# Kernel tuning notes

Measured on AMD Instinct MI355X. Metric: run time of the kernel, lower is better.

Reference implementation:

```python
import jax, jax.numpy as jnp
import numpy as np

B, T, D, H = 4, 2048, 2048, 16
DH = D // H

def setup_inputs() -> dict:
    key = jax.random.key(0)
    ks = jax.random.split(key, 9)
    s = 1.0 / np.sqrt(D)
    return {
        "x": jax.random.normal(ks[0], (B, T, D), dtype=jnp.float32),
        "Wq": jax.random.uniform(ks[1], (D, D), jnp.float32, -s, s),
        "bq": jax.random.uniform(ks[2], (D,), jnp.float32, -s, s),
        "Wk": jax.random.uniform(ks[3], (D, D), jnp.float32, -s, s),
        "bk": jax.random.uniform(ks[4], (D,), jnp.float32, -s, s),
        "Wv": jax.random.uniform(ks[5], (D, D), jnp.float32, -s, s),
        "bv": jax.random.uniform(ks[6], (D,), jnp.float32, -s, s),
        "Wo": jax.random.uniform(ks[7], (D, D), jnp.float32, -s, s),
        "bo": jax.random.uniform(ks[8], (D,), jnp.float32, -s, s),
    }

def reference(x, Wq, bq, Wk, bk, Wv, bv, Wo, bo):
    # projections: [B,T,D] -> [B,H,T,DH]
    def split_heads(y):
        return y.reshape(B, T, H, DH).transpose(0, 2, 1, 3)
    q = split_heads(x @ Wq + bq)
    k = split_heads(x @ Wk + bk)
    v = split_heads(x @ Wv + bv)
    scale = DH ** -0.5
    scores = jnp.einsum('bhtd,bhsd->bhts', q, k) * scale  # [B,H,T,T]
    causal = jnp.tril(jnp.ones((T, T), dtype=bool))
    scores = jnp.where(causal[None, None], scores, -jnp.inf)
    weights = jax.nn.softmax(scores, axis=-1)
    out = jnp.einsum('bhts,bhsd->bhtd', weights, v)  # [B,H,T,DH]
    out = out.transpose(0, 2, 1, 3).reshape(B, T, D)
    return out @ Wo + bo
```

## Files before the change

### kernel.cpp

```cpp
#include <hip/hip_runtime.h>
#include <hip/hip_bf16.h>

#define B_  4
#define T_  2048
#define D_  2048
#define H_  16
#define DH_ 128

typedef __attribute__((ext_vector_type(4))) float f32x4;
typedef __attribute__((ext_vector_type(8))) short short8;
typedef __attribute__((ext_vector_type(4))) _Float16 half4;

__device__ __forceinline__ ushort f2bf(float f) {
    unsigned int u = __builtin_bit_cast(unsigned int, f);
    u += 0x7fffu + ((u >> 16) & 1u);
    return (ushort)(u >> 16);
}
__device__ __forceinline__ ushort f2h(float f) {
    return (ushort)(__builtin_bit_cast(unsigned int, __builtin_amdgcn_cvt_pkrtz(f, f)) & 0xffffu);
}

__device__ __forceinline__ void glds16(const void* g, void* l) {
    __builtin_amdgcn_global_load_lds(
        (const __attribute__((address_space(1))) unsigned int*)g,
        (__attribute__((address_space(3))) unsigned int*)l, 16, 0, 0);
}

__global__ void cast_f32_bf16(const float* __restrict__ x, ushort* __restrict__ xb, int n) {
    int i = (blockIdx.x * 256 + threadIdx.x) * 4;
    if (i < n) {
        float4 v = *(const float4*)(x + i);
        ushort4 o;
        o.x = f2bf(v.x); o.y = f2bf(v.y); o.z = f2bf(v.z); o.w = f2bf(v.w);
        *(ushort4*)(xb + i) = o;
    }
}

__global__ void transpose_cast(const float* __restrict__ W, ushort* __restrict__ Wt) {
    __shared__ float tile[32][33];
    int tx = threadIdx.x, ty = threadIdx.y;
    int n0 = blockIdx.x * 32, k0 = blockIdx.y * 32;
#pragma unroll
    for (int i = 0; i < 4; i++)
        tile[ty + i * 8][tx] = W[(size_t)(k0 + ty + i * 8) * D_ + n0 + tx];
    __syncthreads();
#pragma unroll
    for (int i = 0; i < 4; i++)
        Wt[(size_t)(n0 + ty + i * 8) * D_ + k0 + tx] = f2bf(tile[tx][ty + i * 8]);
}

__global__ __launch_bounds__(256, 3) void gemm_qkv(
    const ushort* __restrict__ A,
    const ushort* __restrict__ Wq, const ushort* __restrict__ Wk, const ushort* __restrict__ Wv,
    const float* __restrict__ bq, const float* __restrict__ bk, const float* __restrict__ bv,
    ushort* __restrict__ Qb, ushort* __restrict__ Kb, ushort* __restrict__ Vtb,
    float qscale)
{
    extern __shared__ char smem[];
    uint4* sA = (uint4*)smem;
    uint4* sB = (uint4*)(smem + 8192);

    const int tid  = threadIdx.x;
    const int sel  = blockIdx.x >> 4;
    const int row0 = blockIdx.y * 128, col0 = (blockIdx.x & 15) * 128;
    const ushort* Bt = (sel == 0) ? Wq : (sel == 1) ? Wk : Wv;
    const float* bias = (sel == 0) ? bq : (sel == 1) ? bk : bv;
    const float oscale = (sel == 0) ? qscale : 1.0f;
    const int K = D_, N = D_;

    const int mA = tid >> 2, g = tid & 3;
    const int gc = g ^ ((mA >> 2) & 3);
    const ushort* pa0 = A  + (size_t)(row0 + mA) * K + gc * 8;
    const ushort* pb0 = Bt + (size_t)(col0 + mA) * K + gc * 8;

    const int lane = tid & 63, w = tid >> 6;
    const int l15 = lane & 15, quad = lane >> 4;
    const int wm = w & 1, wn = w >> 1;
    const int csel = quad ^ ((l15 >> 2) & 3);
    int aoff[4], boff[4];
#pragma unroll
    for (int mt = 0; mt < 4; mt++) aoff[mt] = (wm * 64 + mt * 16 + l15) * 4 + csel;
#pragma unroll
    for (int nt = 0; nt < 4; nt++) boff[nt] = (wn * 64 + nt * 16 + l15) * 4 + csel;

    f32x4 acc[4][4] = {};

    const int kIter = K >> 5;
    for (int kt = 0; kt < kIter; ++kt) {
        if (kt) __syncthreads();
        glds16(pa0 + kt * 32,                     sA + tid);
        glds16(pa0 + kt * 32 + (size_t)64 * K,    sA + tid + 256);
        glds16(pb0 + kt * 32,                     sB + tid);
        glds16(pb0 + kt * 32 + (size_t)64 * K,    sB + tid + 256);
        __syncthreads();
        short8 af[4], bfr[4];
#pragma unroll
        for (int mt = 0; mt < 4; mt++) af[mt]  = __builtin_bit_cast(short8, sA[aoff[mt]]);
#pragma unroll
        for (int nt = 0; nt < 4; nt++) bfr[nt] = __builtin_bit_cast(short8, sB[boff[nt]]);
#pragma unroll
        for (int mt = 0; mt < 4; mt++)
#pragma unroll
            for (int nt = 0; nt < 4; nt++)
                acc[mt][nt] = __builtin_amdgcn_mfma_f32_16x16x32_bf16(af[mt], bfr[nt], acc[mt][nt], 0, 0, 0);
    }

    if (sel < 2) {
        ushort* Cout = (sel == 0) ? Qb : Kb;
#pragma unroll
        for (int nt = 0; nt < 4; nt++) {
            int col = col0 + wn * 64 + nt * 16 + l15;
            float bb = bias[col];
#pragma unroll
            for (int mt = 0; mt < 4; mt++) {
                int rowb = row0 + wm * 64 + mt * 16 + quad * 4;
#pragma unroll
                for (int r = 0; r < 4; r++)
                    Cout[(size_t)(rowb + r) * N + col] = f2bf((acc[mt][nt][r] + bb) * oscale);
            }
        }
    } else {
        __syncthreads();
        ushort* tr = (ushort*)smem;
#pragma unroll
        for (int nt = 0; nt < 4; nt++) {
            int cl = wn * 64 + nt * 16 + l15;
            float bb = bias[col0 + cl];
#pragma unroll
            for (int mt = 0; mt < 4; mt++) {
                int rl = wm * 64 + mt * 16 + quad * 4;
#pragma unroll
                for (int r = 0; r < 4; r++)
                    tr[cl * 136 + rl + r] = f2h(acc[mt][nt][r] + bb);
            }
        }
        __syncthreads();
        int b = row0 >> 11, t0 = row0 & (T_ - 1), h = col0 >> 7;
        for (int idx = tid; idx < 2048; idx += 256) {
            int dh = idx >> 4, c = idx & 15;
            uint4 v = *(const uint4*)(tr + dh * 136 + c * 8);
            *(uint4*)(Vtb + (size_t)((b * H_ + h) * DH_ + dh) * T_ + t0 + c * 8) = v;
        }
    }
}

__global__ __launch_bounds__(256, 3) void gemm_bt_f32(
    const ushort* __restrict__ A, const ushort* __restrict__ Bt,
    const float* __restrict__ bias, float* __restrict__ Cout,
    int M, int N, int K)
{
    extern __shared__ char smem[];
    uint4* sA = (uint4*)smem;
    uint4* sB = (uint4*)(smem + 8192);

    const int tid  = threadIdx.x;
    const int row0 = blockIdx.y * 128, col0 = blockIdx.x * 128;

    const int mA = tid >> 2, g = tid & 3;
    const int gc = g ^ ((mA >> 2) & 3);
    const ushort* pa0 = A  + (size_t)(row0 + mA) * K + gc * 8;
    const ushort* pb0 = Bt + (size_t)(col0 + mA) * K + gc * 8;

    const int lane = tid & 63, w = tid >> 6;
    const int l15 = lane & 15, quad = lane >> 4;
    const int wm = w & 1, wn = w >> 1;
    const int csel = quad ^ ((l15 >> 2) & 3);
    int aoff[4], boff[4];
#pragma unroll
    for (int mt = 0; mt < 4; mt++) aoff[mt] = (wm * 64 + mt * 16 + l15) * 4 + csel;
#pragma unroll
    for (int nt = 0; nt < 4; nt++) boff[nt] = (wn * 64 + nt * 16 + l15) * 4 + csel;

    f32x4 acc[4][4] = {};

    const int kIter = K >> 5;
    for (int kt = 0; kt < kIter; ++kt) {
        if (kt) __syncthreads();
        glds16(pa0 + kt * 32,                     sA + tid);
        glds16(pa0 + kt * 32 + (size_t)64 * K,    sA + tid + 256);
        glds16(pb0 + kt * 32,                     sB + tid);
        glds16(pb0 + kt * 32 + (size_t)64 * K,    sB + tid + 256);
        __syncthreads();
        short8 af[4], bfr[4];
#pragma unroll
        for (int mt = 0; mt < 4; mt++) af[mt]  = __builtin_bit_cast(short8, sA[aoff[mt]]);
#pragma unroll
        for (int nt = 0; nt < 4; nt++) bfr[nt] = __builtin_bit_cast(short8, sB[boff[nt]]);
#pragma unroll
        for (int mt = 0; mt < 4; mt++)
#pragma unroll
            for (int nt = 0; nt < 4; nt++)
                acc[mt][nt] = __builtin_amdgcn_mfma_f32_16x16x32_bf16(af[mt], bfr[nt], acc[mt][nt], 0, 0, 0);
    }

#pragma unroll
    for (int nt = 0; nt < 4; nt++) {
        int col = col0 + wn * 64 + nt * 16 + l15;
        float bb = bias[col];
#pragma unroll
        for (int mt = 0; mt < 4; mt++) {
            int rowb = row0 + wm * 64 + mt * 16 + quad * 4;
#pragma unroll
            for (int r = 0; r < 4; r++)
                Cout[(size_t)(rowb + r) * N + col] = acc[mt][nt][r] + bb;
        }
    }
}

__global__ __launch_bounds__(256, 5) void attn_kernel(
    const ushort* __restrict__ Q, const ushort* __restrict__ K,
    const ushort* __restrict__ Vt, ushort* __restrict__ O)
{
    __shared__ __align__(16) char smem[32768];
    uint4*  kS = (uint4*)smem;
    ushort* vS = (ushort*)(smem + 16384);

    const int tid = threadIdx.x;
    const int bid = blockIdx.x;
    const int slot = bid >> 3;
    const int g = (bid & 7) + 8 * (slot >> 4);
    const int qx = slot & 15;
    const int b = g >> 4, h = g & 15;

    const int lane = tid & 63, w = tid >> 6, l15 = lane & 15, quad = lane >> 4;

    const int krow = tid >> 4;
    const int kchunk = (tid & 15) ^ (krow & 7);
    const ushort* kg = K + ((size_t)(b * T_) + krow) * D_ + h * DH_ + kchunk * 8;

    const int vrow = tid >> 3, vc = tid & 7;
    const ushort* vg = Vt + ((size_t)((b * H_ + h) * DH_) + vrow) * T_ + vc * 8;
    const int vs0 = ((2 * vc    ) ^ (vrow & 15)) * 4;
    const int vs1 = ((2 * vc + 1) ^ (vrow & 15)) * 4;

    const int qts[2] = { qx, 31 - qx };

    for (int e = 0; e < 2; ++e) {
        const int qt = qts[e], q0 = qt * 64;
        const int qbase = q0 + w * 16;

        short8 aq[4];
        {
            const ushort* qp = Q + ((size_t)(b * T_) + qbase + l15) * D_ + h * DH_ + quad * 8;
#pragma unroll
            for (int ks = 0; ks < 4; ++ks)
                aq[ks] = __builtin_bit_cast(short8, *(const uint4*)(qp + ks * 32));
        }

        f32x4 accO[8] = {};
        float mrow = -INFINITY, lrow = 0.f;

        auto tile = [&](int s0, int stMax, bool diag) {
            __syncthreads();
            const ushort* kp = kg + (size_t)s0 * D_;
#pragma unroll
            for (int j = 0; j < 4; ++j) glds16(kp + (size_t)j * 16 * D_, kS + j * 256 + tid);
            const ushort* vp = vg + s0;
            uint4 vv[4];
#pragma unroll
            for (int j = 0; j < 4; ++j) vv[j] = *(const uint4*)(vp + (size_t)j * 32 * T_);
#pragma unroll
            for (int j = 0; j < 4; ++j) {
                ushort* dst = vS + (j * 32 + vrow) * 64;
                *(uint2*)(dst + vs0) = make_uint2(vv[j].x, vv[j].y);
                *(uint2*)(dst + vs1) = make_uint2(vv[j].z, vv[j].w);
            }
            __syncthreads();

            f32x4 sT[4] = {};
#pragma unroll
            for (int ks = 0; ks < 4; ++ks)
#pragma unroll
                for (int st = 0; st < 4; ++st)
                    if (st < stMax) {
                        int row = st * 16 + l15;
                        short8 ak = __builtin_bit_cast(short8, kS[row * 16 + ((ks * 4 + quad) ^ (row & 7))]);
                        sT[st] = __builtin_amdgcn_mfma_f32_16x16x32_bf16(ak, aq[ks], sT[st], 0, 0, 0);
                    }

            if (diag) {
                const int q = qbase + l15;
                const int st = stMax - 1;
#pragma unroll
                for (int r = 0; r < 4; ++r)
                    if (s0 + st * 16 + quad * 4 + r > q) sT[st][r] = -INFINITY;
            }

            float rmax = -INFINITY;
#pragma unroll
            for (int st = 0; st < 4; ++st)
                if (st < stMax)
#pragma unroll
                    for (int r = 0; r < 4; ++r) rmax = fmaxf(rmax, sT[st][r]);
            rmax = fmaxf(rmax, __shfl_xor(rmax, 16));
            rmax = fmaxf(rmax, __shfl_xor(rmax, 32));
            float mnew  = fmaxf(mrow, rmax);
            float alpha = __builtin_amdgcn_exp2f(mrow - mnew);
            mrow = mnew;

            float psum = 0.f;
            half4 pb[4];
#pragma unroll
            for (int st = 0; st < 4; ++st)
                if (st < stMax) {
                    float p0 = __builtin_amdgcn_exp2f(sT[st][0] - mnew);
                    float p1 = __builtin_amdgcn_exp2f(sT[st][1] - mnew);
                    float p2 = __builtin_amdgcn_exp2f(sT[st][2] - mnew);
                    float p3 = __builtin_amdgcn_exp2f(sT[st][3] - mnew);
                    psum += (p0 + p1) + (p2 + p3);
                    uint2 u;
                    u.x = __builtin_bit_cast(unsigned int, __builtin_amdgcn_cvt_pkrtz(p0, p1));
                    u.y = __builtin_bit_cast(unsigned int, __builtin_amdgcn_cvt_pkrtz(p2, p3));
                    pb[st] = __builtin_bit_cast(half4, u);
                }
            psum += __shfl_xor(psum, 16);
            psum += __shfl_xor(psum, 32);
            lrow = lrow * alpha + psum;
#pragma unroll
            for (int nt = 0; nt < 8; ++nt)
#pragma unroll
                for (int r = 0; r < 4; ++r) accO[nt][r] *= alpha;

#pragma unroll
            for (int st = 0; st < 4; ++st)
                if (st < stMax) {
#pragma unroll
                    for (int nt = 0; nt < 8; ++nt) {
                        int dh = nt * 16 + l15;
                        half4 vf = *(const half4*)(vS + dh * 64 + (((st * 4 + quad) ^ l15) * 4));
                        accO[nt] = __builtin_amdgcn_mfma_f32_16x16x16f16(vf, pb[st], accO[nt], 0, 0, 0);
                    }
                }
        };

        for (int it = 0; it < qt; ++it) tile(it * 64, 4, false);
        tile(qt * 64, w + 1, true);

        __syncthreads();
        ushort* eT = (ushort*)smem + w * 2176;
        float inv = 1.0f / lrow;
#pragma unroll
        for (int nt = 0; nt < 8; ++nt) {
            int dh = nt * 16 + quad * 4;
#pragma unroll
            for (int r = 0; r < 4; ++r)
                eT[l15 * 136 + dh + r] = f2bf(accO[nt][r] * inv);
        }
        for (int idx = lane; idx < 256; idx += 64) {
            int row = idx >> 4, c = idx & 15;
            uint4 v = *(const uint4*)(eT + row * 136 + c * 8);
            *(uint4*)(O + ((size_t)(b * T_) + q0 + w * 16 + row) * D_ + h * DH_ + c * 8) = v;
        }
    }
}

extern "C" void kernel_launch(void* const* d_in, const int* in_sizes, int n_in,
                              void* d_out, int out_size, void* d_ws, size_t ws_size,
                              hipStream_t stream) {
    const float* x  = (const float*)d_in[0];
    const float* Wq = (const float*)d_in[1];
    const float* bq = (const float*)d_in[2];
    const float* Wk = (const float*)d_in[3];
    const float* bk = (const float*)d_in[4];
    const float* Wv = (const float*)d_in[5];
    const float* bv = (const float*)d_in[6];
    const float* Wo = (const float*)d_in[7];
    const float* bo = (const float*)d_in[8];

    char* ws = (char*)d_ws;
    const size_t MB = 1u << 20;
    ushort* xb  = (ushort*)(ws);
    ushort* Wqt = (ushort*)(ws + 32 * MB);
    ushort* Wkt = (ushort*)(ws + 40 * MB);
    ushort* Wvt = (ushort*)(ws + 48 * MB);
    ushort* Wot = (ushort*)(ws + 56 * MB);
    ushort* Qb  = (ushort*)(ws + 64 * MB);
    ushort* Kb  = (ushort*)(ws + 96 * MB);
    ushort* Vtb = (ushort*)(ws + 128 * MB);
    ushort* Ob  = (ushort*)(ws + 160 * MB);

    const int M = B_ * T_;
    const float qscale = (float)(0.08838834764831845 * 1.4426950408889634);

    cast_f32_bf16<<<(M * D_) / 1024, 256, 0, stream>>>(x, xb, M * D_);
    dim3 tb(32, 8), tg(D_ / 32, D_ / 32);
    transpose_cast<<<tg, tb, 0, stream>>>(Wq, Wqt);
    transpose_cast<<<tg, tb, 0, stream>>>(Wk, Wkt);
    transpose_cast<<<tg, tb, 0, stream>>>(Wv, Wvt);
    transpose_cast<<<tg, tb, 0, stream>>>(Wo, Wot);

    gemm_qkv<<<dim3(48, M / 128), 256, 34816, stream>>>(
        xb, Wqt, Wkt, Wvt, bq, bk, bv, Qb, Kb, Vtb, qscale);

    attn_kernel<<<dim3(1024), 256, 0, stream>>>(Qb, Kb, Vtb, Ob);

    gemm_bt_f32<<<dim3(D_ / 128, M / 128), 256, 16384, stream>>>(
        Ob, Wot, bo, (float*)d_out, M, D_, D_);
}
```

Measured before the change: 630.5 us.

## Replace QKV and output GEMMs with 256x256 double-buffered pipelined MFMA kernels

```diff
diff --git a/kernel.cpp b/kernel.cpp
--- a/kernel.cpp
+++ b/kernel.cpp
@@ -6,6 +6,7 @@
 #define D_  2048
 #define H_  16
 #define DH_ 128
+#define KG  2048
 
 typedef __attribute__((ext_vector_type(4))) float f32x4;
 typedef __attribute__((ext_vector_type(8))) short short8;
@@ -49,7 +50,84 @@
         Wt[(size_t)(n0 + ty + i * 8) * D_ + k0 + tx] = f2bf(tile[tx][ty + i * 8]);
 }
 
-__global__ __launch_bounds__(256, 3) void gemm_qkv(
+
+#define LDS_A(d, qm, AF)                                                                   \
+  { const char* base_ = smem + (((d)*2 + (qm)) << 14);                                     \
+    _Pragma("unroll") for (int mt = 0; mt < 4; ++mt)                                       \
+      _Pragma("unroll") for (int kk = 0; kk < 2; ++kk) {                                   \
+        int idx_ = wm*64 + mt*16 + l15;                                                    \
+        AF[mt][kk] = __builtin_bit_cast(short8,                                            \
+            *(const uint4*)(base_ + idx_*128 + (((kk*4 + quad) ^ (l15 & 7)) << 4)));       \
+      } }
+
+#define LDS_B(d, qn, BF)                                                                   \
+  { const char* base_ = smem + 65536 + (((d)*2 + (qn)) << 14);                             \
+    _Pragma("unroll") for (int nt = 0; nt < 2; ++nt)                                       \
+      _Pragma("unroll") for (int kk = 0; kk < 2; ++kk) {                                   \
+        int idx_ = wn*32 + nt*16 + l15;                                                    \
+        BF[nt][kk] = __builtin_bit_cast(short8,                                            \
+            *(const uint4*)(base_ + idx_*128 + (((kk*4 + quad) ^ (l15 & 7)) << 4)));       \
+      } }
+
+#define STAGE_A(d, qm, kt)                                                                 \
+  { char* ld_ = smem + (((d)*2 + (qm)) << 14) + tid*16;                                    \
+    const ushort* s_ = Ap + (size_t)(arow + (qm)*64) * KG + (kt)*64 + chl*8;               \
+    glds16(s_, ld_);                                                                       \
+    glds16(s_ + (size_t)128*KG, ld_ + 8192); }
+
+#define STAGE_B(d, qn, kt)                                                                 \
+  { char* ld_ = smem + 65536 + (((d)*2 + (qn)) << 14) + tid*16;                            \
+    const ushort* s_ = Bp + (size_t)(bcol + (qn)*32) * KG + (kt)*64 + chl*8;               \
+    glds16(s_, ld_);                                                                       \
+    glds16(s_ + (size_t)128*KG, ld_ + 8192); }
+
+#define MFMA16(QM, QN, AF, BF)                                                             \
+  __builtin_amdgcn_s_setprio(1);                                                           \
+  _Pragma("unroll") for (int mt = 0; mt < 4; ++mt)                                         \
+    _Pragma("unroll") for (int nt = 0; nt < 2; ++nt)                                       \
+      _Pragma("unroll") for (int kk = 0; kk < 2; ++kk)                                     \
+        acc[(QM)*4 + mt][(QN)*2 + nt] = __builtin_amdgcn_mfma_f32_16x16x32_bf16(           \
+            AF[mt][kk], BF[nt][kk], acc[(QM)*4 + mt][(QN)*2 + nt], 0, 0, 0);               \
+  __builtin_amdgcn_s_setprio(0);
+
+#define BAR1_LGKM  __builtin_amdgcn_s_barrier();                                           \
+                   asm volatile("s_waitcnt lgkmcnt(0)" ::: "memory");
+#define BAR2       __builtin_amdgcn_s_barrier();
+#define VM4        asm volatile("s_waitcnt vmcnt(4)" ::: "memory");
+#define VM0        asm volatile("s_waitcnt vmcnt(0)" ::: "memory");
+
+#define GEMM256_MAIN_LOOP                                                                  \
+    f32x4 acc[8][4] = {};                                                                  \
+    short8 aF[4][2], bF0[2][2], bF1[2][2];                                                 \
+                               \
+    STAGE_B(0, 0, 0); STAGE_A(0, 0, 0); STAGE_A(0, 1, 0); STAGE_B(0, 1, 0);                \
+    STAGE_B(1, 0, 1); STAGE_A(1, 0, 1);                                                    \
+    VM4; __builtin_amdgcn_s_barrier();                                                     \
+    _Pragma("unroll 1")                                                                    \
+    for (int j = 0; j < 16; ++j) {                                                         \
+        const int t1 = 2*j + 1;                                                            \
+        const int t2 = (2*j + 2 < 32) ? 2*j + 2 : 31;                                      \
+        const int t3 = (2*j + 3 < 32) ? 2*j + 3 : 31;                                      \
+         LDS_A(0, 0, aF); LDS_B(0, 0, bF0); STAGE_A(1, 1, t1);                     \
+                 BAR1_LGKM; MFMA16(0, 0, aF, bF0); BAR2;                                   \
+         LDS_B(0, 1, bF1); STAGE_B(1, 1, t1);                                      \
+                 BAR1_LGKM; MFMA16(0, 1, aF, bF1); BAR2;                                   \
+         LDS_A(0, 1, aF); STAGE_B(0, 0, t2);                                       \
+                 BAR1_LGKM; MFMA16(1, 1, aF, bF1); BAR2;                                   \
+         STAGE_A(0, 0, t2);                                                        \
+                 BAR1_LGKM; MFMA16(1, 0, aF, bF0); VM4; BAR2;                              \
+         LDS_A(1, 0, aF); LDS_B(1, 0, bF0); STAGE_A(0, 1, t2);                     \
+                 BAR1_LGKM; MFMA16(0, 0, aF, bF0); BAR2;                                   \
+         LDS_B(1, 1, bF1); STAGE_B(0, 1, t2);                                      \
+                 BAR1_LGKM; MFMA16(0, 1, aF, bF1); BAR2;                                   \
+         LDS_A(1, 1, aF); STAGE_B(1, 0, t3);                                       \
+                 BAR1_LGKM; MFMA16(1, 1, aF, bF1); BAR2;                                   \
+         STAGE_A(1, 0, t3);                                                        \
+                 BAR1_LGKM; MFMA16(1, 0, aF, bF0); VM4; BAR2;                              \
+    }                                                                                      \
+    VM0; __builtin_amdgcn_s_barrier();
+
+__global__ __launch_bounds__(512, 2) void gemm_qkv256(
     const ushort* __restrict__ A,
     const ushort* __restrict__ Wq, const ushort* __restrict__ Wk, const ushort* __restrict__ Wv,
     const float* __restrict__ bq, const float* __restrict__ bk, const float* __restrict__ bv,
@@ -57,152 +135,109 @@
     float qscale)
 {
     extern __shared__ char smem[];
-    uint4* sA = (uint4*)smem;
-    uint4* sB = (uint4*)(smem + 8192);
-
-    const int tid  = threadIdx.x;
-    const int sel  = blockIdx.x >> 4;
-    const int row0 = blockIdx.y * 128, col0 = (blockIdx.x & 15) * 128;
-    const ushort* Bt = (sel == 0) ? Wq : (sel == 1) ? Wk : Wv;
+    const int tid = threadIdx.x;
+
+    int id = blockIdx.y * 24 + blockIdx.x;
+    id = (id & 7) * 96 + (id >> 3);
+    const int bx = id % 24, by = id / 24;
+
+    const int sel  = bx >> 3;
+    const int row0 = by * 256, col0 = (bx & 7) * 256;
+    const ushort* Ap = A;
+    const ushort* Bp = (sel == 0) ? Wq : (sel == 1) ? Wk : Wv;
     const float* bias = (sel == 0) ? bq : (sel == 1) ? bk : bv;
     const float oscale = (sel == 0) ? qscale : 1.0f;
-    const int K = D_, N = D_;
-
-    const int mA = tid >> 2, g = tid & 3;
-    const int gc = g ^ ((mA >> 2) & 3);
-    const ushort* pa0 = A  + (size_t)(row0 + mA) * K + gc * 8;
-    const ushort* pb0 = Bt + (size_t)(col0 + mA) * K + gc * 8;
 
     const int lane = tid & 63, w = tid >> 6;
     const int l15 = lane & 15, quad = lane >> 4;
     const int wm = w & 1, wn = w >> 1;
-    const int csel = quad ^ ((l15 >> 2) & 3);
-    int aoff[4], boff[4];
-#pragma unroll
-    for (int mt = 0; mt < 4; mt++) aoff[mt] = (wm * 64 + mt * 16 + l15) * 4 + csel;
-#pragma unroll
-    for (int nt = 0; nt < 4; nt++) boff[nt] = (wn * 64 + nt * 16 + l15) * 4 + csel;
-
-    f32x4 acc[4][4] = {};
-
-    const int kIter = K >> 5;
-    for (int kt = 0; kt < kIter; ++kt) {
-        if (kt) __syncthreads();
-        glds16(pa0 + kt * 32,                     sA + tid);
-        glds16(pa0 + kt * 32 + (size_t)64 * K,    sA + tid + 256);
-        glds16(pb0 + kt * 32,                     sB + tid);
-        glds16(pb0 + kt * 32 + (size_t)64 * K,    sB + tid + 256);
-        __syncthreads();
-        short8 af[4], bfr[4];
-#pragma unroll
-        for (int mt = 0; mt < 4; mt++) af[mt]  = __builtin_bit_cast(short8, sA[aoff[mt]]);
-#pragma unroll
-        for (int nt = 0; nt < 4; nt++) bfr[nt] = __builtin_bit_cast(short8, sB[boff[nt]]);
-#pragma unroll
-        for (int mt = 0; mt < 4; mt++)
-#pragma unroll
-            for (int nt = 0; nt < 4; nt++)
-                acc[mt][nt] = __builtin_amdgcn_mfma_f32_16x16x32_bf16(af[mt], bfr[nt], acc[mt][nt], 0, 0, 0);
+
+    const int irow = tid >> 3;
+    const int chl  = (tid & 7) ^ (irow & 7);
+    const int arow = row0 + irow;
+    const int bcol = col0 + ((irow >> 5) << 6) + (irow & 31);
+
+    GEMM256_MAIN_LOOP
+
+    if (sel < 2) {
+        ushort* Cout = sel ? Kb : Qb;
+#pragma unroll
+        for (int ntg = 0; ntg < 4; ++ntg) {
+            int col = col0 + wn * 64 + ntg * 16 + l15;
+            float bb = bias[col];
+#pragma unroll
+            for (int mtg = 0; mtg < 8; ++mtg) {
+                int rowb = row0 + wm * 128 + mtg * 16 + quad * 4;
+#pragma unroll
+                for (int r = 0; r < 4; ++r)
+                    Cout[(size_t)(rowb + r) * D_ + col] = f2bf((acc[mtg][ntg][r] + bb) * oscale);
+            }
+        }
+    } else {
+        const int b = row0 >> 11, t0 = (row0 & (T_ - 1)) + wm * 128;
+        const int h = (col0 + wn * 64) >> 7;
+        ushort* eT = (ushort*)smem + w * (32 * 136);
+#pragma unroll 1
+        for (int rnd = 0; rnd < 2; ++rnd) {
+#pragma unroll
+            for (int ni = 0; ni < 2; ++ni) {
+                int ntg = rnd * 2 + ni;
+                int col = col0 + wn * 64 + ntg * 16 + l15;
+                float bb = bias[col];
+#pragma unroll
+                for (int mtg = 0; mtg < 8; ++mtg)
+#pragma unroll
+                    for (int r = 0; r < 4; ++r)
+                        eT[(ni * 16 + l15) * 136 + mtg * 16 + quad * 4 + r] = f2h(acc[mtg][ntg][r] + bb);
+            }
+            int dhbase = ((wn & 1) ? 64 : 0) + rnd * 32;
+#pragma unroll
+            for (int it = 0; it < 8; ++it) {
+                int chunk = it * 64 + lane;
+                int d2 = chunk >> 4, c = chunk & 15;
+                uint4 v = *(const uint4*)(eT + d2 * 136 + c * 8);
+                *(uint4*)(Vtb + (size_t)((b * H_ + h) * DH_ + dhbase + d2) * T_ + t0 + c * 8) = v;
+            }
+        }
     }
-
-    if (sel < 2) {
-        ushort* Cout = (sel == 0) ? Qb : Kb;
-#pragma unroll
-        for (int nt = 0; nt < 4; nt++) {
-            int col = col0 + wn * 64 + nt * 16 + l15;
-            float bb = bias[col];
-#pragma unroll
-            for (int mt = 0; mt < 4; mt++) {
-                int rowb = row0 + wm * 64 + mt * 16 + quad * 4;
-#pragma unroll
-                for (int r = 0; r < 4; r++)
-                    Cout[(size_t)(rowb + r) * N + col] = f2bf((acc[mt][nt][r] + bb) * oscale);
-            }
-        }
-    } else {
-        __syncthreads();
-        ushort* tr = (ushort*)smem;
-#pragma unroll
-        for (int nt = 0; nt < 4; nt++) {
-            int cl = wn * 64 + nt * 16 + l15;
-            float bb = bias[col0 + cl];
-#pragma unroll
-            for (int mt = 0; mt < 4; mt++) {
-                int rl = wm * 64 + mt * 16 + quad * 4;
-#pragma unroll
-                for (int r = 0; r < 4; r++)
-                    tr[cl * 136 + rl + r] = f2h(acc[mt][nt][r] + bb);
-            }
-        }
-        __syncthreads();
-        int b = row0 >> 11, t0 = row0 & (T_ - 1), h = col0 >> 7;
-        for (int idx = tid; idx < 2048; idx += 256) {
-            int dh = idx >> 4, c = idx & 15;
-            uint4 v = *(const uint4*)(tr + dh * 136 + c * 8);
-            *(uint4*)(Vtb + (size_t)((b * H_ + h) * DH_ + dh) * T_ + t0 + c * 8) = v;
-        }
-    }
-}
-
-__global__ __launch_bounds__(256, 3) void gemm_bt_f32(
+}
+
+__global__ __launch_bounds__(512, 2) void gemm_o256(
     const ushort* __restrict__ A, const ushort* __restrict__ Bt,
-    const float* __restrict__ bias, float* __restrict__ Cout,
-    int M, int N, int K)
+    const float* __restrict__ bias, float* __restrict__ Cout)
 {
     extern __shared__ char smem[];
-    uint4* sA = (uint4*)smem;
-    uint4* sB = (uint4*)(smem + 8192);
-
-    const int tid  = threadIdx.x;
-    const int row0 = blockIdx.y * 128, col0 = blockIdx.x * 128;
-
-    const int mA = tid >> 2, g = tid & 3;
-    const int gc = g ^ ((mA >> 2) & 3);
-    const ushort* pa0 = A  + (size_t)(row0 + mA) * K + gc * 8;
-    const ushort* pb0 = Bt + (size_t)(col0 + mA) * K + gc * 8;
+    const int tid = threadIdx.x;
+
+    int id = blockIdx.y * 8 + blockIdx.x;
+    id = (id & 7) * 32 + (id >> 3);
+    const int bx = id % 8, by = id / 8;
+
+    const int row0 = by * 256, col0 = bx * 256;
+    const ushort* Ap = A;
+    const ushort* Bp = Bt;
 
     const int lane = tid & 63, w = tid >> 6;
     const int l15 = lane & 15, quad = lane >> 4;
     const int wm = w & 1, wn = w >> 1;
-    const int csel = quad ^ ((l15 >> 2) & 3);
-    int aoff[4], boff[4];
-#pragma unroll
-    for (int mt = 0; mt < 4; mt++) aoff[mt] = (wm * 64 + mt * 16 + l15) * 4 + csel;
-#pragma unroll
-    for (int nt = 0; nt < 4; nt++) boff[nt] = (wn * 64 + nt * 16 + l15) * 4 + csel;
-
-    f32x4 acc[4][4] = {};
-
-    const int kIter = K >> 5;
-    for (int kt = 0; kt < kIter; ++kt) {
-        if (kt) __syncthreads();
-        glds16(pa0 + kt * 32,                     sA + tid);
-        glds16(pa0 + kt * 32 + (size_t)64 * K,    sA + tid + 256);
-        glds16(pb0 + kt * 32,                     sB + tid);
-        glds16(pb0 + kt * 32 + (size_t)64 * K,    sB + tid + 256);
-        __syncthreads();
-        short8 af[4], bfr[4];
-#pragma unroll
-        for (int mt = 0; mt < 4; mt++) af[mt]  = __builtin_bit_cast(short8, sA[aoff[mt]]);
-#pragma unroll
-        for (int nt = 0; nt < 4; nt++) bfr[nt] = __builtin_bit_cast(short8, sB[boff[nt]]);
-#pragma unroll
-        for (int mt = 0; mt < 4; mt++)
-#pragma unroll
-            for (int nt = 0; nt < 4; nt++)
-                acc[mt][nt] = __builtin_amdgcn_mfma_f32_16x16x32_bf16(af[mt], bfr[nt], acc[mt][nt], 0, 0, 0);
-    }
-
-#pragma unroll
-    for (int nt = 0; nt < 4; nt++) {
-        int col = col0 + wn * 64 + nt * 16 + l15;
+
+    const int irow = tid >> 3;
+    const int chl  = (tid & 7) ^ (irow & 7);
+    const int arow = row0 + irow;
+    const int bcol = col0 + ((irow >> 5) << 6) + (irow & 31);
+
+    GEMM256_MAIN_LOOP
+
+#pragma unroll
+    for (int ntg = 0; ntg < 4; ++ntg) {
+        int col = col0 + wn * 64 + ntg * 16 + l15;
         float bb = bias[col];
 #pragma unroll
-        for (int mt = 0; mt < 4; mt++) {
-            int rowb = row0 + wm * 64 + mt * 16 + quad * 4;
-#pragma unroll
-            for (int r = 0; r < 4; r++)
-                Cout[(size_t)(rowb + r) * N + col] = acc[mt][nt][r] + bb;
+        for (int mtg = 0; mtg < 8; ++mtg) {
+            int rowb = row0 + wm * 128 + mtg * 16 + quad * 4;
+#pragma unroll
+            for (int r = 0; r < 4; ++r)
+                Cout[(size_t)(rowb + r) * D_ + col] = acc[mtg][ntg][r] + bb;
         }
     }
 }
@@ -382,6 +417,15 @@
     const int M = B_ * T_;
     const float qscale = (float)(0.08838834764831845 * 1.4426950408889634);
 
+    static bool attr_done = false;
+    if (!attr_done) {
+        (void)hipFuncSetAttribute((const void*)gemm_qkv256,
+                                  hipFuncAttributeMaxDynamicSharedMemorySize, 131072);
+        (void)hipFuncSetAttribute((const void*)gemm_o256,
+                                  hipFuncAttributeMaxDynamicSharedMemorySize, 131072);
+        attr_done = true;
+    }
+
     cast_f32_bf16<<<(M * D_) / 1024, 256, 0, stream>>>(x, xb, M * D_);
     dim3 tb(32, 8), tg(D_ / 32, D_ / 32);
     transpose_cast<<<tg, tb, 0, stream>>>(Wq, Wqt);
@@ -389,11 +433,11 @@
     transpose_cast<<<tg, tb, 0, stream>>>(Wv, Wvt);
     transpose_cast<<<tg, tb, 0, stream>>>(Wo, Wot);
 
-    gemm_qkv<<<dim3(48, M / 128), 256, 34816, stream>>>(
+    gemm_qkv256<<<dim3(24, M / 256), 512, 131072, stream>>>(
         xb, Wqt, Wkt, Wvt, bq, bk, bv, Qb, Kb, Vtb, qscale);
 
     attn_kernel<<<dim3(1024), 256, 0, stream>>>(Qb, Kb, Vtb, Ob);
 
-    gemm_bt_f32<<<dim3(D_ / 128, M / 128), 256, 16384, stream>>>(
-        Ob, Wot, bo, (float*)d_out, M, D_, D_);
-}
+    gemm_o256<<<dim3(D_ / 256, M / 256), 512, 131072, stream>>>(
+        Ob, Wot, bo, (float*)d_out);
+}
```

After: 680.4 us. 7.9% more time.
